# Performance work log

Measured on AMD Instinct MI355X. Metric: run time of the kernel, lower is better.

## Reference

```python
import jax, jax.numpy as jnp
import numpy as np

C_IN = 128
C_OUT = 128
C4 = C_IN // 4  # 32
PX, PY = 8, 8
B, H, W = 4, 256, 256


def gelu(v):
    return jax.nn.gelu(v, approximate=False)  # torch nn.GELU default (erf)


def conv2d(v, w, b, groups=1):
    p = (w.shape[-1] - 1) // 2
    y = jax.lax.conv_general_dilated(v, w, (1, 1), [(p, p), (p, p)],
                                     dimension_numbers=('NCHW', 'OIHW', 'NCHW'),
                                     feature_group_count=groups)
    return y + b[None, :, None, None]


def conv1d(v, w, b, groups=1):
    p = (w.shape[-1] - 1) // 2
    y = jax.lax.conv_general_dilated(v, w, (1,), [(p, p)],
                                     dimension_numbers=('NCH', 'OIH', 'NCH'),
                                     feature_group_count=groups)
    return y + b[None, :, None]


def ln_cf(v, w, b, eps=1e-6):
    # channels_first LayerNorm over axis 1 (ConvNeXt style)
    u = jnp.mean(v, axis=1, keepdims=True)
    s = jnp.mean((v - u) ** 2, axis=1, keepdims=True)
    v = (v - u) / jnp.sqrt(s + eps)
    return w[:, None, None] * v + b[:, None, None]


def interp_last(p, out):
    # bilinear, align_corners=True, along last axis
    L = p.shape[-1]
    if out == 1:
        return p[..., :1]
    coords = jnp.arange(out, dtype=p.dtype) * ((L - 1) / (out - 1))
    i0 = jnp.clip(jnp.floor(coords).astype(jnp.int32), 0, L - 1)
    i1 = jnp.clip(i0 + 1, 0, L - 1)
    wgt = coords - i0.astype(p.dtype)
    return jnp.take(p, i0, axis=-1) * (1 - wgt) + jnp.take(p, i1, axis=-1) * wgt


def setup_inputs() -> dict:
    key = jax.random.key(0)
    ks = jax.random.split(key, 20)
    sd = 0.05
    d = {
        'x': jax.random.normal(ks[0], (B, C_IN, H, W), jnp.float32),
        'norm1_w': jnp.ones((C_IN,), jnp.float32),
        'norm1_b': jnp.zeros((C_IN,), jnp.float32),
        'params_xy': jnp.ones((1, C4, PX, PY), jnp.float32),
        'cxy_dw_w': jax.random.normal(ks[1], (C4, 1, 3, 3), jnp.float32) * sd,
        'cxy_dw_b': jnp.zeros((C4,), jnp.float32),
        'cxy_pw_w': jax.random.normal(ks[2], (C4, C4, 1, 1), jnp.float32) * sd,
        'cxy_pw_b': jnp.zeros((C4,), jnp.float32),
        'params_zx': jnp.ones((1, 1, C4, PX), jnp.float32),
        'czx_dw_w': jax.random.normal(ks[3], (C4, 1, 3), jnp.float32) * sd,
        'czx_dw_b': jnp.zeros((C4,), jnp.float32),
        'czx_pw_w': jax.random.normal(ks[4], (C4, C4, 1), jnp.float32) * sd,
        'czx_pw_b': jnp.zeros((C4,), jnp.float32),
        'params_zy': jnp.ones((1, 1, C4, PY), jnp.float32),
        'czy_dw_w': jax.random.normal(ks[5], (C4, 1, 3), jnp.float32) * sd,
        'czy_dw_b': jnp.zeros((C4,), jnp.float32),
        'czy_pw_w': jax.random.normal(ks[6], (C4, C4, 1), jnp.float32) * sd,
        'czy_pw_b': jnp.zeros((C4,), jnp.float32),
        'dw_pw_w': jax.random.normal(ks[7], (C4, C4, 1, 1), jnp.float32) * sd,
        'dw_pw_b': jnp.zeros((C4,), jnp.float32),
        'dw_dw_w': jax.random.normal(ks[8], (C4, 1, 3, 3), jnp.float32) * sd,
        'dw_dw_b': jnp.zeros((C4,), jnp.float32),
        'norm2_w': jnp.ones((C_IN,), jnp.float32),
        'norm2_b': jnp.zeros((C_IN,), jnp.float32),
        'ldw_dw_w': jax.random.normal(ks[9], (C_IN, 1, 3, 3), jnp.float32) * sd,
        'ldw_dw_b': jnp.zeros((C_IN,), jnp.float32),
        'ldw_pw_w': jax.random.normal(ks[10], (C_OUT, C_IN, 1, 1), jnp.float32) * sd,
        'ldw_pw_b': jnp.zeros((C_OUT,), jnp.float32),
    }
    return d


def reference(x, norm1_w, norm1_b, params_xy, cxy_dw_w, cxy_dw_b, cxy_pw_w, cxy_pw_b,
              params_zx, czx_dw_w, czx_dw_b, czx_pw_w, czx_pw_b,
              params_zy, czy_dw_w, czy_dw_b, czy_pw_w, czy_pw_b,
              dw_pw_w, dw_pw_b, dw_dw_w, dw_dw_b, norm2_w, norm2_b,
              ldw_dw_w, ldw_dw_b, ldw_pw_w, ldw_pw_b):
    x = ln_cf(x, norm1_w, norm1_b)
    res = x
    c = x.shape[1] // 4
    x1, x2, x3, x4 = jnp.split(x, 4, axis=1)
    Bn, _, Hn, Wn = x1.shape
    # --- xy branch: 2D bilinear(align_corners) of [1,c,PX,PY] -> [1,c,H,W]
    p = interp_last(params_xy, Wn)  # interp W
    p = jnp.swapaxes(interp_last(jnp.swapaxes(p, -2, -1), Hn), -2, -1)  # interp H
    att_xy = conv2d(gelu(conv2d(p, cxy_dw_w, cxy_dw_b, groups=c)), cxy_pw_w, cxy_pw_b)
    x1 = x1 * att_xy
    # --- zx branch: operate on [B,W,c,H]
    x2p = jnp.transpose(x2, (0, 3, 1, 2))
    # interpolate [1,1,c,PX] -> (c,H): c->c is identity under align_corners
    pz = interp_last(params_zx, Hn)[0]  # [1,c,H]
    att_zx = conv1d(gelu(conv1d(pz, czx_dw_w, czx_dw_b, groups=c)), czx_pw_w, czx_pw_b)[None]  # [1,1,c,H]
    x2 = jnp.transpose(x2p * att_zx, (0, 2, 3, 1))
    # --- zy branch: operate on [B,H,c,W]
    x3p = jnp.transpose(x3, (0, 2, 1, 3))
    py = interp_last(params_zy, Wn)[0]  # [1,c,W]
    att_zy = conv1d(gelu(conv1d(py, czy_dw_w, czy_dw_b, groups=c)), czy_pw_w, czy_pw_b)[None]
    x3 = jnp.transpose(x3p * att_zy, (0, 2, 1, 3))
    # --- dw branch: 1x1 -> GELU -> depthwise 3x3
    x4 = conv2d(gelu(conv2d(x4, dw_pw_w, dw_pw_b)), dw_dw_w, dw_dw_b, groups=c)
    x = jnp.concatenate([x1, x2, x3, x4], axis=1)
    x = ln_cf(x, norm2_w, norm2_b) + res
    # ldw: depthwise 3x3 -> GELU -> 1x1 to dim_out
    x = conv2d(gelu(conv2d(x, ldw_dw_w, ldw_dw_b, groups=x.shape[1])), ldw_pw_w, ldw_pw_b)
    return x
```

## Files before the change

kernel.cpp:

```cpp
#include <hip/hip_runtime.h>
#include <hip/hip_bf16.h>
#include <math.h>

#define HH 256
#define WW 256
#define NB 4
#define NC 128
#define C4 32

typedef __attribute__((ext_vector_type(8))) short short8v;
typedef __attribute__((ext_vector_type(4))) float float4v;
typedef unsigned short ushort_t;

__device__ __forceinline__ float gelu_f(float v) {
    return 0.5f * v * (1.0f + erff(v * 0.7071067811865476f));
}
__device__ __forceinline__ unsigned short f2bf(float x) {
    __hip_bfloat16 h = __float2bfloat16(x);
    return __builtin_bit_cast(unsigned short, h);
}
__device__ __forceinline__ float bf2f(unsigned short u) {
    return __uint_as_float(((unsigned)u) << 16);
}
__device__ __forceinline__ float bfe(short8v v, int j) {
    return bf2f((ushort_t)v[j]);
}

__global__ void attxy_kernel(const float* __restrict__ params,
                             const float* __restrict__ dww, const float* __restrict__ dwb,
                             const float* __restrict__ pww, const float* __restrict__ pwb,
                             ushort_t* __restrict__ att)
{
    __shared__ float P[2048];
    __shared__ float DW[288];
    __shared__ float PW[1024];
    for (int i = threadIdx.x; i < 2048; i += 256) P[i] = params[i];
    for (int i = threadIdx.x; i < 288;  i += 256) DW[i] = dww[i];
    for (int i = threadIdx.x; i < 1024; i += 256) PW[i] = pww[i];
    __syncthreads();
    const int idx = blockIdx.x * 256 + threadIdx.x;
    const int h = idx >> 8, w = idx & 255;

    int iy0[3], iy1[3], ix0[3], ix1[3];
    float fy[3], fx[3];
    bool vy[3], vx[3];
#pragma unroll
    for (int d = 0; d < 3; ++d) {
        int hh = h - 1 + d;
        vy[d] = (hh >= 0 && hh < HH);
        float cy = hh * (7.0f / 255.0f);
        int i0 = (int)floorf(cy); i0 = min(max(i0, 0), 7);
        iy0[d] = i0; iy1[d] = min(i0 + 1, 7); fy[d] = cy - (float)i0;
        int ww2 = w - 1 + d;
        vx[d] = (ww2 >= 0 && ww2 < WW);
        float cx = ww2 * (7.0f / 255.0f);
        int j0 = (int)floorf(cx); j0 = min(max(j0, 0), 7);
        ix0[d] = j0; ix1[d] = min(j0 + 1, 7); fx[d] = cx - (float)j0;
    }
    float g[32];
#pragma unroll
    for (int c = 0; c < 32; ++c) {
        float a = dwb[c];
        const float* Pc = P + c * 64;
#pragma unroll
        for (int dy = 0; dy < 3; ++dy) {
            if (!vy[dy]) continue;
#pragma unroll
            for (int dx = 0; dx < 3; ++dx) {
                if (!vx[dx]) continue;
                float p00 = Pc[iy0[dy] * 8 + ix0[dx]];
                float p01 = Pc[iy0[dy] * 8 + ix1[dx]];
                float p10 = Pc[iy1[dy] * 8 + ix0[dx]];
                float p11 = Pc[iy1[dy] * 8 + ix1[dx]];
                float pt = p00 + (p01 - p00) * fx[dx];
                float pb = p10 + (p11 - p10) * fx[dx];
                float p  = pt + (pb - pt) * fy[dy];
                a += DW[c * 9 + dy * 3 + dx] * p;
            }
        }
        g[c] = gelu_f(a);
    }
    ushort_t* ap = att + (size_t)idx * 32;
#pragma unroll
    for (int q = 0; q < 4; ++q) {
        short8v pk;
#pragma unroll
        for (int j = 0; j < 8; ++j) {
            const int co = q * 8 + j;
            float a = pwb[co];
#pragma unroll
            for (int c = 0; c < 32; ++c) a += PW[co * 32 + c] * g[c];
            pk[j] = (short)f2bf(a);
        }
        *(short8v*)(ap + q * 8) = pk;
    }
}

__global__ void attz_kernel(const float* __restrict__ params_zx, const float* __restrict__ zx_dww,
                            const float* __restrict__ zx_dwb, const float* __restrict__ zx_pww,
                            const float* __restrict__ zx_pwb,
                            const float* __restrict__ params_zy, const float* __restrict__ zy_dww,
                            const float* __restrict__ zy_dwb, const float* __restrict__ zy_pww,
                            const float* __restrict__ zy_pwb,
                            float* __restrict__ att_zx, float* __restrict__ att_zy)
{
    const bool sel = (blockIdx.x != 0);
    const float* params = sel ? params_zy : params_zx;
    const float* dww = sel ? zy_dww : zx_dww;
    const float* dwb = sel ? zy_dwb : zx_dwb;
    const float* pww = sel ? zy_pww : zx_pww;
    const float* pwb = sel ? zy_pwb : zx_pwb;
    float* att = sel ? att_zy : att_zx;
    const int pos = threadIdx.x;
    float g[32];
#pragma unroll
    for (int c = 0; c < 32; ++c) {
        float a = dwb[c];
#pragma unroll
        for (int d = 0; d < 3; ++d) {
            int p = pos - 1 + d;
            if (p < 0 || p > 255) continue;
            float cz = p * (7.0f / 255.0f);
            int i0 = (int)floorf(cz); i0 = min(max(i0, 0), 7);
            int i1 = min(i0 + 1, 7);
            float f = cz - (float)i0;
            float pv = params[c * 8 + i0];
            pv += (params[c * 8 + i1] - pv) * f;
            a += dww[c * 3 + d] * pv;
        }
        g[c] = gelu_f(a);
    }
#pragma unroll
    for (int co = 0; co < 32; ++co) {
        float a = pwb[co];
#pragma unroll
        for (int ci = 0; ci < 32; ++ci) a += pww[co * 32 + ci] * g[ci];
        att[co * 256 + pos] = a;
    }
}

__global__ void convert_pw_kernel(const float* __restrict__ pw, ushort_t* __restrict__ pwb16) {
    int i = blockIdx.x * 256 + threadIdx.x;
    pwb16[i] = f2bf(pw[i]);
}

__global__ void convert_ldwdw_kernel(const float* __restrict__ dww, ushort_t* __restrict__ dwwT) {
    int i = blockIdx.x * 256 + threadIdx.x;
    if (i < 1152) {
        int c = i / 9, tap = i % 9;
        dwwT[tap * 128 + c] = f2bf(dww[i]);
    }
}

__global__ __launch_bounds__(256, 3) void ln1g_kernel(
    const float* __restrict__ x,
    const float* __restrict__ n1w, const float* __restrict__ n1b,
    const float* __restrict__ pww, const float* __restrict__ pwb,
    ushort_t* __restrict__ g, float2* __restrict__ stats)
{
    const int b = blockIdx.x >> 8, h = blockIdx.x & 255, w = threadIdx.x;
    const int pix = h * WW + w;
    const float* xp = x + (size_t)b * NC * 65536 + pix;

    float s1 = 0.f, s2 = 0.f;
    float x4v[32];
#pragma unroll
    for (int k = 0; k < 96; ++k) {
        float v = xp[(size_t)k * 65536];
        s1 += v; s2 += v * v;
    }
#pragma unroll
    for (int j = 0; j < 32; ++j) {
        float v = xp[(size_t)(96 + j) * 65536];
        x4v[j] = v; s1 += v; s2 += v * v;
    }
    const float m = s1 * (1.f / 128.f);
    const float r = rsqrtf(s2 * (1.f / 128.f) - m * m + 1e-6f);
    stats[(size_t)b * 65536 + pix] = float2{m, r};

#pragma unroll
    for (int j = 0; j < 32; ++j)
        x4v[j] = (x4v[j] - m) * r * n1w[96 + j] + n1b[96 + j];

    ushort_t* gp = g + ((size_t)b * 65536 + pix) * 32;
#pragma unroll
    for (int q = 0; q < 4; ++q) {
        short8v pk;
#pragma unroll
        for (int j = 0; j < 8; ++j) {
            const int co = q * 8 + j;
            float a = pwb[co];
#pragma unroll
            for (int jj = 0; jj < 32; ++jj) a += pww[co * 32 + jj] * x4v[jj];
            pk[j] = (short)f2bf(gelu_f(a));
        }
        *(short8v*)(gp + q * 8) = pk;
    }
}

__global__ __launch_bounds__(256) void fuse_kernel(
    const float* __restrict__ x, const float2* __restrict__ stats,
    const float* __restrict__ n1w, const float* __restrict__ n1b,
    const float* __restrict__ n2w, const float* __restrict__ n2b,
    const ushort_t* __restrict__ att_xy, const float* __restrict__ att_zx,
    const float* __restrict__ att_zy,
    const ushort_t* __restrict__ g,
    const float* __restrict__ dww, const float* __restrict__ dwb,
    ushort_t* __restrict__ z)
{
    __shared__ __align__(16) ushort_t gs[3][66][40];
    __shared__ float rs[4][64];
    __shared__ float rq[4][64];

    const int lid  = (blockIdx.x & 7) * 512 + (blockIdx.x >> 3);
    const int b     = lid >> 10;
    const int h     = (lid >> 2) & 255;
    const int strip = lid & 3;
    const int tid = threadIdx.x;
    const int q  = tid >> 6;
    const int px = tid & 63;
    const int w  = strip * 64 + px;
    const int pix = h * WW + w;
    const int w0g = strip * 64;

    for (int i = tid; i < 792; i += 256) {
        const int row  = i / 264;
        const int rem  = i % 264;
        const int colc = rem >> 2;
        const int q8   = rem & 3;
        const int hy = min(max(h - 1 + row, 0), 255);
        const int cg = min(max(w0g + colc - 1, 0), 255);
        const short8v v = *(const short8v*)(g + ((size_t)b * 65536 + hy * WW + cg) * 32 + q8 * 8);
        *(short8v*)&gs[row][colc][q8 * 8] = v;
    }
    __syncthreads();

    const float2 st = stats[(size_t)b * 65536 + pix];
    const float m1 = st.x, r1 = st.y;

    float xn[4][8], u[4][8];
    {
        const short8v av = *(const short8v*)(att_xy + (size_t)pix * 32 + q * 8);
#pragma unroll
        for (int j = 0; j < 8; ++j) {
            const int c = q * 8 + j;
            float xv = x[((size_t)(b * NC + c)) * 65536 + pix];
            float v = (xv - m1) * r1 * n1w[c] + n1b[c];
            xn[0][j] = v; u[0][j] = v * bfe(av, j);
        }
    }
#pragma unroll
    for (int j = 0; j < 8; ++j) {
        const int c = 32 + q * 8 + j;
        float xv = x[((size_t)(b * NC + c)) * 65536 + pix];
        float v = (xv - m1) * r1 * n1w[c] + n1b[c];
        xn[1][j] = v; u[1][j] = v * att_zx[(c - 32) * 256 + h];
    }
#pragma unroll
    for (int j = 0; j < 8; ++j) {
        const int c = 64 + q * 8 + j;
        float xv = x[((size_t)(b * NC + c)) * 65536 + pix];
        float v = (xv - m1) * r1 * n1w[c] + n1b[c];
        xn[2][j] = v; u[2][j] = v * att_zy[(c - 64) * 256 + w];
    }
    {
        float a[8];
#pragma unroll
        for (int j = 0; j < 8; ++j) a[j] = dwb[q * 8 + j];
        const float ml = (w > 0) ? 1.f : 0.f;
        const float mr = (w < 255) ? 1.f : 0.f;
#pragma unroll
        for (int dy = -1; dy <= 1; ++dy) {
            int hy = h + dy;
            if (hy < 0 || hy > 255) continue;
            const int rr = dy + 1;
            short8v gl = *(const short8v*)&gs[rr][px][q * 8];
            short8v gc = *(const short8v*)&gs[rr][px + 1][q * 8];
            short8v gv = *(const short8v*)&gs[rr][px + 2][q * 8];
            const int r0 = rr * 3;
#pragma unroll
            for (int j = 0; j < 8; ++j) {
                const float* wk = dww + (q * 8 + j) * 9 + r0;
                a[j] += (wk[0] * ml) * bfe(gl, j);
                a[j] += wk[1] * bfe(gc, j);
                a[j] += (wk[2] * mr) * bfe(gv, j);
            }
        }
#pragma unroll
        for (int j = 0; j < 8; ++j) {
            const int c = 96 + q * 8 + j;
            float xv = x[((size_t)(b * NC + c)) * 65536 + pix];
            xn[3][j] = (xv - m1) * r1 * n1w[c] + n1b[c];
            u[3][j] = a[j];
        }
    }
    float e1 = 0.f, e2 = 0.f;
#pragma unroll
    for (int br = 0; br < 4; ++br)
#pragma unroll
        for (int j = 0; j < 8; ++j) { e1 += u[br][j]; e2 += u[br][j] * u[br][j]; }
    rs[q][px] = e1; rq[q][px] = e2;
    __syncthreads();
    const float ssum = rs[0][px] + rs[1][px] + rs[2][px] + rs[3][px];
    const float qsum = rq[0][px] + rq[1][px] + rq[2][px] + rq[3][px];
    const float m2 = ssum * (1.f / 128.f);
    const float r2 = rsqrtf(qsum * (1.f / 128.f) - m2 * m2 + 1e-6f);
    ushort_t* zp = z + ((size_t)b * 65536 + pix) * 128;
#pragma unroll
    for (int br = 0; br < 4; ++br) {
        short8v pk;
#pragma unroll
        for (int j = 0; j < 8; ++j) {
            const int c = br * 32 + q * 8 + j;
            pk[j] = (short)f2bf((u[br][j] - m2) * r2 * n2w[c] + n2b[c] + xn[br][j]);
        }
        *(short8v*)(zp + br * 32 + q * 8) = pk;
    }
}

__global__ __launch_bounds__(256, 3) void ldw_kernel(
    const ushort_t* __restrict__ z, const ushort_t* __restrict__ dwwT,
    const float* __restrict__ dwb, const ushort_t* __restrict__ wb16,
    const float* __restrict__ pwb, float* __restrict__ out)
{
    __shared__ __align__(16) ushort_t tl[64 * 128];

    const int lid  = (blockIdx.x & 7) * 512 + (blockIdx.x >> 3);
    const int b    = lid >> 10;
    const int h    = (lid >> 2) & 255;
    const int px0  = (lid & 3) * 64;
    const int tid  = threadIdx.x;

    {
        const int oc = tid & 15;
        const int pr = tid >> 4;
        short8v wt[9];
#pragma unroll
        for (int t = 0; t < 9; ++t)
            wt[t] = *(const short8v*)(dwwT + t * 128 + oc * 8);
        const float4 bd0 = *(const float4*)(dwb + oc * 8);
        const float4 bd1 = *(const float4*)(dwb + oc * 8 + 4);
        const float bdw[8] = {bd0.x, bd0.y, bd0.z, bd0.w, bd1.x, bd1.y, bd1.z, bd1.w};
        char* tlb = (char*)tl;
#pragma unroll
        for (int it = 0; it < 4; ++it) {
            const int px = it * 16 + pr;
            const int w  = px0 + px;
            const int wl = (w > 0) ? w - 1 : 0;
            const int wr2 = (w < 255) ? w + 1 : 255;
            const float ml = (w > 0) ? 1.f : 0.f;
            const float mr = (w < 255) ? 1.f : 0.f;
            float a[8];
#pragma unroll
            for (int j = 0; j < 8; ++j) a[j] = bdw[j];
#pragma unroll
            for (int dy = -1; dy <= 1; ++dy) {
                int hy = h + dy;
                if (hy < 0 || hy > 255) continue;
                const ushort_t* zr = z + ((size_t)b * 65536 + hy * WW) * 128 + oc * 8;
                short8v vl = *(const short8v*)(zr + (size_t)wl * 128);
                short8v vc = *(const short8v*)(zr + (size_t)w * 128);
                short8v vr = *(const short8v*)(zr + (size_t)wr2 * 128);
                const int r0 = (dy + 1) * 3;
#pragma unroll
                for (int j = 0; j < 8; ++j) {
                    a[j] += (bfe(wt[r0], j) * ml) * bfe(vl, j);
                    a[j] += bfe(wt[r0 + 1], j) * bfe(vc, j);
                    a[j] += (bfe(wt[r0 + 2], j) * mr) * bfe(vr, j);
                }
            }
            short8v pk;
#pragma unroll
            for (int j = 0; j < 8; ++j) pk[j] = (short)f2bf(gelu_f(a[j]));
            const int chunk = oc ^ (px & 15);
            *(short8v*)(tlb + px * 256 + chunk * 16) = pk;
        }
    }
    __syncthreads();

    const int lane = tid & 63;
    const int wv   = tid >> 6;
    const int l15  = lane & 15;
    const int l4   = lane >> 4;

    short8v afrag[2][4];
#pragma unroll
    for (int ct = 0; ct < 2; ++ct) {
        const int co = wv * 32 + ct * 16 + l15;
#pragma unroll
        for (int ks = 0; ks < 4; ++ks)
            afrag[ct][ks] = *(const short8v*)(wb16 + co * 128 + ks * 32 + l4 * 8);
    }
    float4v bias[2];
#pragma unroll
    for (int ct = 0; ct < 2; ++ct) {
        const float4 bv = *(const float4*)(pwb + wv * 32 + ct * 16 + l4 * 4);
        bias[ct] = float4v{bv.x, bv.y, bv.z, bv.w};
    }

    const char* tlb = (const char*)tl;
#pragma unroll
    for (int pt = 0; pt < 4; ++pt) {
        const int px = pt * 16 + l15;
        short8v bfrag[4];
#pragma unroll
        for (int ks = 0; ks < 4; ++ks) {
            const int chunk = (ks * 4 + l4) ^ (px & 15);
            bfrag[ks] = *(const short8v*)(tlb + px * 256 + chunk * 16);
        }
        float4v acc0 = bias[0];
        float4v acc1 = bias[1];
#pragma unroll
        for (int ks = 0; ks < 4; ++ks) {
            acc0 = __builtin_amdgcn_mfma_f32_16x16x32_bf16(afrag[0][ks], bfrag[ks], acc0, 0, 0, 0);
            acc1 = __builtin_amdgcn_mfma_f32_16x16x32_bf16(afrag[1][ks], bfrag[ks], acc1, 0, 0, 0);
        }
#pragma unroll
        for (int ct = 0; ct < 2; ++ct) {
            const int co = wv * 32 + ct * 16 + l4 * 4;
            float* op = out + ((size_t)(b * NC + co)) * 65536 + h * WW + px0 + pt * 16 + l15;
            const float4v av = ct ? acc1 : acc0;
#pragma unroll
            for (int r = 0; r < 4; ++r) op[(size_t)r * 65536] = av[r];
        }
    }
}

extern "C" void kernel_launch(void* const* d_in, const int* in_sizes, int n_in,
                              void* d_out, int out_size, void* d_ws, size_t ws_size,
                              hipStream_t stream)
{
    (void)in_sizes; (void)n_in; (void)out_size; (void)ws_size;
    const float* x       = (const float*)d_in[0];
    const float* n1w     = (const float*)d_in[1];
    const float* n1b     = (const float*)d_in[2];
    const float* pxy     = (const float*)d_in[3];
    const float* cxy_dww = (const float*)d_in[4];
    const float* cxy_dwb = (const float*)d_in[5];
    const float* cxy_pww = (const float*)d_in[6];
    const float* cxy_pwb = (const float*)d_in[7];
    const float* pzx     = (const float*)d_in[8];
    const float* czx_dww = (const float*)d_in[9];
    const float* czx_dwb = (const float*)d_in[10];
    const float* czx_pww = (const float*)d_in[11];
    const float* czx_pwb = (const float*)d_in[12];
    const float* pzy     = (const float*)d_in[13];
    const float* czy_dww = (const float*)d_in[14];
    const float* czy_dwb = (const float*)d_in[15];
    const float* czy_pww = (const float*)d_in[16];
    const float* czy_pwb = (const float*)d_in[17];
    const float* dw_pww  = (const float*)d_in[18];
    const float* dw_pwb  = (const float*)d_in[19];
    const float* dw_dww  = (const float*)d_in[20];
    const float* dw_dwb  = (const float*)d_in[21];
    const float* n2w     = (const float*)d_in[22];
    const float* n2b     = (const float*)d_in[23];
    const float* ldw_dww = (const float*)d_in[24];
    const float* ldw_dwb = (const float*)d_in[25];
    const float* ldw_pww = (const float*)d_in[26];
    const float* ldw_pwb = (const float*)d_in[27];
    float* out = (float*)d_out;
    char* ws   = (char*)d_ws;

    ushort_t* att_xy = (ushort_t*)ws;
    float* att_zx = (float*)(ws + 4194304);
    float* att_zy = att_zx + 32 * 256;
    ushort_t* pwb16 = (ushort_t*)(att_zy + 32 * 256);
    ushort_t* dwwT  = pwb16 + 128 * 128;
    ushort_t* gbuf  = dwwT + 2048;
    ushort_t* zbuf  = gbuf + (size_t)4 * 65536 * 32;
    float2* stats   = (float2*)(zbuf + (size_t)4 * 65536 * 128);

    attxy_kernel<<<256, 256, 0, stream>>>(pxy, cxy_dww, cxy_dwb, cxy_pww, cxy_pwb, att_xy);
    attz_kernel<<<2, 256, 0, stream>>>(pzx, czx_dww, czx_dwb, czx_pww, czx_pwb,
                                       pzy, czy_dww, czy_dwb, czy_pww, czy_pwb,
                                       att_zx, att_zy);
    convert_pw_kernel<<<64, 256, 0, stream>>>(ldw_pww, pwb16);
    convert_ldwdw_kernel<<<5, 256, 0, stream>>>(ldw_dww, dwwT);
    ln1g_kernel<<<1024, 256, 0, stream>>>(x, n1w, n1b, dw_pww, dw_pwb, gbuf, stats);
    fuse_kernel<<<4096, 256, 0, stream>>>(x, stats, n1w, n1b, n2w, n2b,
                                          att_xy, att_zx, att_zy,
                                          gbuf, dw_dww, dw_dwb, zbuf);
    ldw_kernel<<<4096, 256, 0, stream>>>(zbuf, dwwT, ldw_dwb, pwb16, ldw_pwb, out);
}
```

Baseline: 269.4 us.

## Merge prep kernels into one launch and hoist x loads before halo staging

Four small setup kernels (att_xy, att_z, and two weight conversions) are merged into a single block-indexed prep kernel, removing three launches. In the fuse kernel, the stats and x channel loads and the normalization of branches 0-3 are moved ahead of the shared-memory halo fill and barrier, so global loads can overlap the staging. This raises live registers across the barrier and may lower occupancy.

```diff
diff --git a/kernel.cpp b/kernel.cpp
--- a/kernel.cpp
+++ b/kernel.cpp
@@ -26,19 +26,79 @@
     return bf2f((ushort_t)v[j]);
 }
 
-__global__ void attxy_kernel(const float* __restrict__ params,
-                             const float* __restrict__ dww, const float* __restrict__ dwb,
-                             const float* __restrict__ pww, const float* __restrict__ pwb,
-                             ushort_t* __restrict__ att)
+__global__ __launch_bounds__(256) void prep_kernel(
+    const float* __restrict__ pxy,
+    const float* __restrict__ cxy_dww, const float* __restrict__ cxy_dwb,
+    const float* __restrict__ cxy_pww, const float* __restrict__ cxy_pwb,
+    const float* __restrict__ pzx, const float* __restrict__ zx_dww,
+    const float* __restrict__ zx_dwb, const float* __restrict__ zx_pww,
+    const float* __restrict__ zx_pwb,
+    const float* __restrict__ pzy, const float* __restrict__ zy_dww,
+    const float* __restrict__ zy_dwb, const float* __restrict__ zy_pww,
+    const float* __restrict__ zy_pwb,
+    const float* __restrict__ ldw_pww, const float* __restrict__ ldw_dww,
+    ushort_t* __restrict__ att_xy, float* __restrict__ att_zx,
+    float* __restrict__ att_zy, ushort_t* __restrict__ pwb16,
+    ushort_t* __restrict__ dwwT)
 {
+    const int bid = blockIdx.x;
+    if (bid >= 258) {
+        if (bid < 322) {
+            int i = (bid - 258) * 256 + threadIdx.x;
+            pwb16[i] = f2bf(ldw_pww[i]);
+        } else {
+            int i = (bid - 322) * 256 + threadIdx.x;
+            if (i < 1152) {
+                int c = i / 9, tap = i % 9;
+                dwwT[tap * 128 + c] = f2bf(ldw_dww[i]);
+            }
+        }
+        return;
+    }
+    if (bid >= 256) {
+        const bool sel = (bid != 256);
+        const float* params = sel ? pzy : pzx;
+        const float* dww = sel ? zy_dww : zx_dww;
+        const float* dwb = sel ? zy_dwb : zx_dwb;
+        const float* pww = sel ? zy_pww : zx_pww;
+        const float* pwb = sel ? zy_pwb : zx_pwb;
+        float* att = sel ? att_zy : att_zx;
+        const int pos = threadIdx.x;
+        float g[32];
+#pragma unroll
+        for (int c = 0; c < 32; ++c) {
+            float a = dwb[c];
+#pragma unroll
+            for (int d = 0; d < 3; ++d) {
+                int p = pos - 1 + d;
+                if (p < 0 || p > 255) continue;
+                float cz = p * (7.0f / 255.0f);
+                int i0 = (int)floorf(cz); i0 = min(max(i0, 0), 7);
+                int i1 = min(i0 + 1, 7);
+                float f = cz - (float)i0;
+                float pv = params[c * 8 + i0];
+                pv += (params[c * 8 + i1] - pv) * f;
+                a += dww[c * 3 + d] * pv;
+            }
+            g[c] = gelu_f(a);
+        }
+#pragma unroll
+        for (int co = 0; co < 32; ++co) {
+            float a = pwb[co];
+#pragma unroll
+            for (int ci = 0; ci < 32; ++ci) a += pww[co * 32 + ci] * g[ci];
+            att[co * 256 + pos] = a;
+        }
+        return;
+    }
     __shared__ float P[2048];
     __shared__ float DW[288];
     __shared__ float PW[1024];
-    for (int i = threadIdx.x; i < 2048; i += 256) P[i] = params[i];
-    for (int i = threadIdx.x; i < 288;  i += 256) DW[i] = dww[i];
-    for (int i = threadIdx.x; i < 1024; i += 256) PW[i] = pww[i];
+    for (int i = threadIdx.x; i < 2048; i += 256) P[i] = pxy[i];
+    for (int i = threadIdx.x; i < 288;  i += 256) DW[i] = cxy_dww[i];
+    for (int i = threadIdx.x; i < 1024; i += 256) PW[i] = cxy_pww[i];
     __syncthreads();
-    const int idx = blockIdx.x * 256 + threadIdx.x;
+    const int idx = bid * 256 + threadIdx.x;
     const int h = idx >> 8, w = idx & 255;
 
     int iy0[3], iy1[3], ix0[3], ix1[3];
@@ -60,7 +120,7 @@
     float g[32];
 #pragma unroll
     for (int c = 0; c < 32; ++c) {
-        float a = dwb[c];
+        float a = cxy_dwb[c];
         const float* Pc = P + c * 64;
 #pragma unroll
         for (int dy = 0; dy < 3; ++dy) {
@@ -80,75 +140,19 @@
         }
         g[c] = gelu_f(a);
     }
-    ushort_t* ap = att + (size_t)idx * 32;
+    ushort_t* ap = att_xy + (size_t)idx * 32;
 #pragma unroll
     for (int q = 0; q < 4; ++q) {
         short8v pk;
 #pragma unroll
         for (int j = 0; j < 8; ++j) {
             const int co = q * 8 + j;
-            float a = pwb[co];
+            float a = cxy_pwb[co];
 #pragma unroll
             for (int c = 0; c < 32; ++c) a += PW[co * 32 + c] * g[c];
             pk[j] = (short)f2bf(a);
         }
         *(short8v*)(ap + q * 8) = pk;
-    }
-}
-
-__global__ void attz_kernel(const float* __restrict__ params_zx, const float* __restrict__ zx_dww,
-                            const float* __restrict__ zx_dwb, const float* __restrict__ zx_pww,
-                            const float* __restrict__ zx_pwb,
-                            const float* __restrict__ params_zy, const float* __restrict__ zy_dww,
-                            const float* __restrict__ zy_dwb, const float* __restrict__ zy_pww,
-                            const float* __restrict__ zy_pwb,
-                            float* __restrict__ att_zx, float* __restrict__ att_zy)
-{
-    const bool sel = (blockIdx.x != 0);
-    const float* params = sel ? params_zy : params_zx;
-    const float* dww = sel ? zy_dww : zx_dww;
-    const float* dwb = sel ? zy_dwb : zx_dwb;
-    const float* pww = sel ? zy_pww : zx_pww;
-    const float* pwb = sel ? zy_pwb : zx_pwb;
-    float* att = sel ? att_zy : att_zx;
-    const int pos = threadIdx.x;
-    float g[32];
-#pragma unroll
-    for (int c = 0; c < 32; ++c) {
-        float a = dwb[c];
-#pragma unroll
-        for (int d = 0; d < 3; ++d) {
-            int p = pos - 1 + d;
-            if (p < 0 || p > 255) continue;
-            float cz = p * (7.0f / 255.0f);
-            int i0 = (int)floorf(cz); i0 = min(max(i0, 0), 7);
-            int i1 = min(i0 + 1, 7);
-            float f = cz - (float)i0;
-            float pv = params[c * 8 + i0];
-            pv += (params[c * 8 + i1] - pv) * f;
-            a += dww[c * 3 + d] * pv;
-        }
-        g[c] = gelu_f(a);
-    }
-#pragma unroll
-    for (int co = 0; co < 32; ++co) {
-        float a = pwb[co];
-#pragma unroll
-        for (int ci = 0; ci < 32; ++ci) a += pww[co * 32 + ci] * g[ci];
-        att[co * 256 + pos] = a;
-    }
-}
-
-__global__ void convert_pw_kernel(const float* __restrict__ pw, ushort_t* __restrict__ pwb16) {
-    int i = blockIdx.x * 256 + threadIdx.x;
-    pwb16[i] = f2bf(pw[i]);
-}
-
-__global__ void convert_ldwdw_kernel(const float* __restrict__ dww, ushort_t* __restrict__ dwwT) {
-    int i = blockIdx.x * 256 + threadIdx.x;
-    if (i < 1152) {
-        int c = i / 9, tap = i % 9;
-        dwwT[tap * 128 + c] = f2bf(dww[i]);
     }
 }
 
@@ -223,6 +227,41 @@
     const int pix = h * WW + w;
     const int w0g = strip * 64;
 
+    const float2 st = stats[(size_t)b * 65536 + pix];
+    const float m1 = st.x, r1 = st.y;
+
+    float xn[4][8], u[4][8];
+    {
+        const short8v av = *(const short8v*)(att_xy + (size_t)pix * 32 + q * 8);
+#pragma unroll
+        for (int j = 0; j < 8; ++j) {
+            const int c = q * 8 + j;
+            float xv = x[((size_t)(b * NC + c)) * 65536 + pix];
+            float v = (xv - m1) * r1 * n1w[c] + n1b[c];
+            xn[0][j] = v; u[0][j] = v * bfe(av, j);
+        }
+    }
+#pragma unroll
+    for (int j = 0; j < 8; ++j) {
+        const int c = 32 + q * 8 + j;
+        float xv = x[((size_t)(b * NC + c)) * 65536 + pix];
+        float v = (xv - m1) * r1 * n1w[c] + n1b[c];
+        xn[1][j] = v; u[1][j] = v * att_zx[(c - 32) * 256 + h];
+    }
+#pragma unroll
+    for (int j = 0; j < 8; ++j) {
+        const int c = 64 + q * 8 + j;
+        float xv = x[((size_t)(b * NC + c)) * 65536 + pix];
+        float v = (xv - m1) * r1 * n1w[c] + n1b[c];
+        xn[2][j] = v; u[2][j] = v * att_zy[(c - 64) * 256 + w];
+    }
+#pragma unroll
+    for (int j = 0; j < 8; ++j) {
+        const int c = 96 + q * 8 + j;
+        float xv = x[((size_t)(b * NC + c)) * 65536 + pix];
+        xn[3][j] = (xv - m1) * r1 * n1w[c] + n1b[c];
+    }
+
     for (int i = tid; i < 792; i += 256) {
         const int row  = i / 264;
         const int rem  = i % 264;
@@ -235,34 +274,6 @@
     }
     __syncthreads();
 
-    const float2 st = stats[(size_t)b * 65536 + pix];
-    const float m1 = st.x, r1 = st.y;
-
-    float xn[4][8], u[4][8];
-    {
-        const short8v av = *(const short8v*)(att_xy + (size_t)pix * 32 + q * 8);
-#pragma unroll
-        for (int j = 0; j < 8; ++j) {
-            const int c = q * 8 + j;
-            float xv = x[((size_t)(b * NC + c)) * 65536 + pix];
-            float v = (xv - m1) * r1 * n1w[c] + n1b[c];
-            xn[0][j] = v; u[0][j] = v * bfe(av, j);
-        }
-    }
-#pragma unroll
-    for (int j = 0; j < 8; ++j) {
-        const int c = 32 + q * 8 + j;
-        float xv = x[((size_t)(b * NC + c)) * 65536 + pix];
-        float v = (xv - m1) * r1 * n1w[c] + n1b[c];
-        xn[1][j] = v; u[1][j] = v * att_zx[(c - 32) * 256 + h];
-    }
-#pragma unroll
-    for (int j = 0; j < 8; ++j) {
-        const int c = 64 + q * 8 + j;
-        float xv = x[((size_t)(b * NC + c)) * 65536 + pix];
-        float v = (xv - m1) * r1 * n1w[c] + n1b[c];
-        xn[2][j] = v; u[2][j] = v * att_zy[(c - 64) * 256 + w];
-    }
     {
         float a[8];
 #pragma unroll
@@ -287,12 +298,7 @@
             }
         }
 #pragma unroll
-        for (int j = 0; j < 8; ++j) {
-            const int c = 96 + q * 8 + j;
-            float xv = x[((size_t)(b * NC + c)) * 65536 + pix];
-            xn[3][j] = (xv - m1) * r1 * n1w[c] + n1b[c];
-            u[3][j] = a[j];
-        }
+        for (int j = 0; j < 8; ++j) u[3][j] = a[j];
     }
     float e1 = 0.f, e2 = 0.f;
 #pragma unroll
@@ -471,12 +477,11 @@
     ushort_t* zbuf  = gbuf + (size_t)4 * 65536 * 32;
     float2* stats   = (float2*)(zbuf + (size_t)4 * 65536 * 128);
 
-    attxy_kernel<<<256, 256, 0, stream>>>(pxy, cxy_dww, cxy_dwb, cxy_pww, cxy_pwb, att_xy);
-    attz_kernel<<<2, 256, 0, stream>>>(pzx, czx_dww, czx_dwb, czx_pww, czx_pwb,
-                                       pzy, czy_dww, czy_dwb, czy_pww, czy_pwb,
-                                       att_zx, att_zy);
-    convert_pw_kernel<<<64, 256, 0, stream>>>(ldw_pww, pwb16);
-    convert_ldwdw_kernel<<<5, 256, 0, stream>>>(ldw_dww, dwwT);
+    prep_kernel<<<327, 256, 0, stream>>>(pxy, cxy_dww, cxy_dwb, cxy_pww, cxy_pwb,
+                                         pzx, czx_dww, czx_dwb, czx_pww, czx_pwb,
+                                         pzy, czy_dww, czy_dwb, czy_pww, czy_pwb,
+                                         ldw_pww, ldw_dww,
+                                         att_xy, att_zx, att_zy, pwb16, dwwT);
     ln1g_kernel<<<1024, 256, 0, stream>>>(x, n1w, n1b, dw_pww, dw_pwb, gbuf, stats);
     fuse_kernel<<<4096, 256, 0, stream>>>(x, stats, n1w, n1b, n2w, n2b,
                                           att_xy, att_zx, att_zy,
```

Result: faster. 231.4 us (-14.1%).
